# Kernel optimization log

Measured on AMD Instinct MI355X. Metric: run time of the kernel, lower is better.

Reference implementation:

```python
import jax, jax.numpy as jnp
import numpy as np

DIM = 1024
HEADS = 16
D_HEAD = 64
INNER = HEADS * D_HEAD  # 1024
CTX_DIM = 768
FF_INNER = 4 * DIM  # 4096
EPS = 1e-5
SCALE = D_HEAD ** -0.5


def _layer_norm(x, g, b):
    m = jnp.mean(x, axis=-1, keepdims=True)
    v = jnp.mean(jnp.square(x - m), axis=-1, keepdims=True)
    return (x - m) * jax.lax.rsqrt(v + EPS) * g + b


def _attention(x, ctx, wq, wk, wv, wo, bo):
    B, S, _ = x.shape
    T = ctx.shape[1]
    # project and split heads -> [B, H, S, Dh]
    q = (x @ wq).reshape(B, S, HEADS, D_HEAD).transpose(0, 2, 1, 3)
    k = (ctx @ wk).reshape(B, T, HEADS, D_HEAD).transpose(0, 2, 1, 3)
    v = (ctx @ wv).reshape(B, T, HEADS, D_HEAD).transpose(0, 2, 1, 3)
    attn = jnp.einsum('bhid,bhjd->bhij', q, k) * SCALE
    attn = jax.nn.softmax(attn, axis=-1)
    out = jnp.einsum('bhij,bhjd->bhid', attn, v)  # [B, H, S, Dh]
    out = out.transpose(0, 2, 1, 3).reshape(B, S, INNER)
    return out @ wo + bo


def setup_inputs() -> dict:
    key = jax.random.key(0)
    ks = jax.random.split(key, 20)
    rn = lambda k, shape, s=0.02: jax.random.normal(k, shape, dtype=jnp.float32) * s
    inp = {
        'hidden_states': jax.random.normal(ks[0], (4, 2048, DIM), dtype=jnp.float32),
        'context': jax.random.normal(ks[1], (4, 77, CTX_DIM), dtype=jnp.float32),
        # self-attention
        'wq1': rn(ks[2], (DIM, INNER)), 'wk1': rn(ks[3], (DIM, INNER)),
        'wv1': rn(ks[4], (DIM, INNER)),
        'wo1': rn(ks[5], (INNER, DIM)), 'bo1': jnp.zeros((DIM,), jnp.float32),
        # cross-attention (k/v from context dim 768)
        'wq2': rn(ks[6], (DIM, INNER)), 'wk2': rn(ks[7], (CTX_DIM, INNER)),
        'wv2': rn(ks[8], (CTX_DIM, INNER)),
        'wo2': rn(ks[9], (INNER, DIM)), 'bo2': jnp.zeros((DIM,), jnp.float32),
        # GEGLU feed-forward
        'w_ff1': rn(ks[10], (DIM, 2 * FF_INNER)), 'b_ff1': jnp.zeros((2 * FF_INNER,), jnp.float32),
        'w_ff2': rn(ks[11], (FF_INNER, DIM)), 'b_ff2': jnp.zeros((DIM,), jnp.float32),
        # layer norms
        'ln1_g': jnp.ones((DIM,), jnp.float32), 'ln1_b': jnp.zeros((DIM,), jnp.float32),
        'ln2_g': jnp.ones((DIM,), jnp.float32), 'ln2_b': jnp.zeros((DIM,), jnp.float32),
        'ln3_g': jnp.ones((DIM,), jnp.float32), 'ln3_b': jnp.zeros((DIM,), jnp.float32),
    }
    return inp


def reference(hidden_states, context, wq1, wk1, wv1, wo1, bo1,
              wq2, wk2, wv2, wo2, bo2, w_ff1, b_ff1, w_ff2, b_ff2,
              ln1_g, ln1_b, ln2_g, ln2_b, ln3_g, ln3_b):
    # self-attention, pre-norm residual
    h = hidden_states
    h = h + _attention(_layer_norm(h, ln1_g, ln1_b), _layer_norm(h, ln1_g, ln1_b),
                       wq1, wk1, wv1, wo1, bo1)
    # cross-attention
    h = h + _attention(_layer_norm(h, ln2_g, ln2_b), context,
                       wq2, wk2, wv2, wo2, bo2)
    # GEGLU feed-forward
    x = _layer_norm(h, ln3_g, ln3_b) @ w_ff1 + b_ff1
    lin, gate = jnp.split(x, 2, axis=2)
    h = h + (lin * jax.nn.gelu(gate)) @ w_ff2 + b_ff2
    return h
```

## Files before the change

### kernel.cpp

```cpp
#include <hip/hip_runtime.h>

#define DIMM 1024
#define NHEADS 16
#define DHEAD 64
#define BATCH 4
#define SEQ 2048
#define TCTX 77
#define CTXD 768
#define FFI 4096

typedef float f32x4 __attribute__((ext_vector_type(4)));
typedef __bf16 bf16x8 __attribute__((ext_vector_type(8)));

__device__ __forceinline__ float bf2f(unsigned short u){
  union { unsigned int i; float f; } c; c.i = ((unsigned int)u) << 16; return c.f;
}
__device__ __forceinline__ unsigned short f2bf(float f){
  union { float f; unsigned int i; } c; c.f = f;
  unsigned int i = c.i;
  return (unsigned short)((i + 0x7fffu + ((i >> 16) & 1u)) >> 16);
}
__device__ __forceinline__ void cp16(const unsigned short* g, unsigned short* l){
  __builtin_amdgcn_global_load_lds(
      (const __attribute__((address_space(1))) unsigned int*)g,
      (__attribute__((address_space(3))) unsigned int*)l, 16, 0, 0);
}

__global__ __launch_bounds__(256) void ln_kernel(const float* __restrict__ x,
                                                 const float* __restrict__ g,
                                                 const float* __restrict__ bb,
                                                 unsigned short* __restrict__ y)
{
  int row = blockIdx.x, tid = threadIdx.x;
  float4 raw = ((const float4*)(x + (size_t)row * DIMM))[tid];
  float v0 = raw.x, v1 = raw.y, v2 = raw.z, v3 = raw.w;
  float s  = v0 + v1 + v2 + v3;
  float sq = v0*v0 + v1*v1 + v2*v2 + v3*v3;
  #pragma unroll
  for (int off = 32; off; off >>= 1){ s += __shfl_xor(s, off); sq += __shfl_xor(sq, off); }
  __shared__ float sm[8];
  int wave = tid >> 6, lane = tid & 63;
  if (lane == 0){ sm[wave] = s; sm[4 + wave] = sq; }
  __syncthreads();
  s  = sm[0] + sm[1] + sm[2] + sm[3];
  sq = sm[4] + sm[5] + sm[6] + sm[7];
  float mean = s * (1.f / DIMM);
  float var  = sq * (1.f / DIMM) - mean * mean;
  float rstd = rsqrtf(var + 1e-5f);
  float4 gr = ((const float4*)g)[tid];
  float4 br = ((const float4*)bb)[tid];
  ushort4 o;
  o.x = f2bf((v0 - mean) * rstd * gr.x + br.x);
  o.y = f2bf((v1 - mean) * rstd * gr.y + br.y);
  o.z = f2bf((v2 - mean) * rstd * gr.z + br.z);
  o.w = f2bf((v3 - mean) * rstd * gr.w + br.w);
  ((ushort4*)(y + (size_t)row * DIMM))[tid] = o;
}

__global__ __launch_bounds__(256) void wt_kernel(const float* __restrict__ in,
                                                 unsigned short* __restrict__ out,
                                                 int K, int N)
{
  __shared__ float t[32][33];
  int tx = threadIdx.x & 31, ty = threadIdx.x >> 5;
  int k0 = blockIdx.y * 32, n0 = blockIdx.x * 32;
  #pragma unroll
  for (int i = 0; i < 4; i++)
    t[ty + i * 8][tx] = in[(size_t)(k0 + ty + i * 8) * N + n0 + tx];
  __syncthreads();
  #pragma unroll
  for (int i = 0; i < 4; i++)
    out[(size_t)(n0 + ty + i * 8) * K + k0 + tx] = f2bf(t[tx][ty + i * 8]);
}

#define CTXE (TCTX * BATCH * CTXD)
__global__ __launch_bounds__(256) void ctxcvt_kernel(const float* __restrict__ in,
                                                     unsigned short* __restrict__ out)
{
  int e = (blockIdx.x * 256 + threadIdx.x) * 4;
  float4 v;
  if (e < CTXE) v = *(const float4*)(in + e);
  else { v.x = 0.f; v.y = 0.f; v.z = 0.f; v.w = 0.f; }
  ushort4 o; o.x = f2bf(v.x); o.y = f2bf(v.y); o.z = f2bf(v.z); o.w = f2bf(v.w);
  *(ushort4*)(out + e) = o;
}

template<int RESF, int CF32>
__global__ __launch_bounds__(256) void gemm_bt(
    const unsigned short* __restrict__ A, int lda,
    const unsigned short* __restrict__ Bt, int ldb,
    const float* __restrict__ bias, const void* __restrict__ resv,
    void* __restrict__ Cv, int ldc,
    int M, int N, int K)
{
  __shared__ __align__(16) unsigned short As[128][64];
  __shared__ __align__(16) unsigned short Bs[128][64];
  int tid = threadIdx.x;
  int n0 = blockIdx.x * 128, row0 = blockIdx.y * 128;
  int wave = tid >> 6, lane = tid & 63, quad = lane >> 4, l16 = lane & 15;
  int wm = (wave >> 1) * 64, wn = (wave & 1) * 64;
  int wrow = wave * 32;
  int lrow = lane >> 3, lgrp = lane & 7;
  int gcol = ((lgrp ^ lrow) * 8);

  f32x4 acc[4][4];
  #pragma unroll
  for (int mt = 0; mt < 4; mt++)
    #pragma unroll
    for (int nt = 0; nt < 4; nt++) acc[mt][nt] = 0.f;

  for (int k0 = 0; k0 < K; k0 += 64) {
    const unsigned short* ga = A  + (size_t)(row0 + wrow + lrow) * lda + k0 + gcol;
    const unsigned short* gb = Bt + (size_t)(n0  + wrow + lrow) * ldb + k0 + gcol;
    #pragma unroll
    for (int i = 0; i < 4; i++){
      cp16(ga + (size_t)(8 * i) * lda, &As[wrow + 8 * i][0]);
      cp16(gb + (size_t)(8 * i) * ldb, &Bs[wrow + 8 * i][0]);
    }
    __syncthreads();
    #pragma unroll
    for (int kc = 0; kc < 2; kc++){
      bf16x8 af[4], bf[4];
      #pragma unroll
      for (int mt = 0; mt < 4; mt++){
        int R = wm + mt * 16 + l16;
        af[mt] = *(const bf16x8*)&As[R][((kc * 4 + quad) ^ (R & 7)) * 8];
      }
      #pragma unroll
      for (int nt = 0; nt < 4; nt++){
        int R = wn + nt * 16 + l16;
        bf[nt] = *(const bf16x8*)&Bs[R][((kc * 4 + quad) ^ (R & 7)) * 8];
      }
      #pragma unroll
      for (int mt = 0; mt < 4; mt++)
        #pragma unroll
        for (int nt = 0; nt < 4; nt++)
          acc[mt][nt] = __builtin_amdgcn_mfma_f32_16x16x32_bf16(af[mt], bf[nt], acc[mt][nt], 0, 0, 0);
    }
    __syncthreads();
  }

  #pragma unroll
  for (int nt = 0; nt < 4; nt++){
    int c = n0 + wn + nt * 16 + l16;
    float bv = bias ? bias[c] : 0.f;
    #pragma unroll
    for (int mt = 0; mt < 4; mt++){
      int rbase = row0 + wm + mt * 16 + quad * 4;
      #pragma unroll
      for (int rr = 0; rr < 4; rr++){
        int r = rbase + rr;
        if (r < M) {
          float val = acc[mt][nt][rr] + bv;
          size_t idx = (size_t)r * ldc + c;
          if (RESF) val += ((const float*)resv)[idx];
          if (CF32) ((float*)Cv)[idx] = val;
          else      ((unsigned short*)Cv)[idx] = f2bf(val);
        }
      }
    }
  }
}

__global__ __launch_bounds__(256) void ff1_geglu_bt(
    const unsigned short* __restrict__ A,
    const unsigned short* __restrict__ BtW,
    const float* __restrict__ bias,
    unsigned short* __restrict__ Z, int M)
{
  __shared__ __align__(16) unsigned short As[128][64];
  __shared__ __align__(16) unsigned short BsL[128][64];
  __shared__ __align__(16) unsigned short BsG[128][64];
  int tid = threadIdx.x;
  int n0 = blockIdx.x * 128, row0 = blockIdx.y * 128;
  int wave = tid >> 6, lane = tid & 63, quad = lane >> 4, l16 = lane & 15;
  int wm = (wave >> 1) * 64, wn = (wave & 1) * 64;
  int wrow = wave * 32;
  int lrow = lane >> 3, lgrp = lane & 7;
  int gcol = ((lgrp ^ lrow) * 8);

  f32x4 accL[4][4], accG[4][4];
  #pragma unroll
  for (int mt = 0; mt < 4; mt++)
    #pragma unroll
    for (int nt = 0; nt < 4; nt++){ accL[mt][nt] = 0.f; accG[mt][nt] = 0.f; }

  for (int k0 = 0; k0 < DIMM; k0 += 64) {
    const unsigned short* ga = A   + (size_t)(row0 + wrow + lrow) * DIMM + k0 + gcol;
    const unsigned short* gl = BtW + (size_t)(n0  + wrow + lrow) * DIMM + k0 + gcol;
    const unsigned short* gg = BtW + (size_t)(FFI + n0 + wrow + lrow) * DIMM + k0 + gcol;
    #pragma unroll
    for (int i = 0; i < 4; i++){
      cp16(ga + (size_t)(8 * i) * DIMM, &As[wrow + 8 * i][0]);
      cp16(gl + (size_t)(8 * i) * DIMM, &BsL[wrow + 8 * i][0]);
      cp16(gg + (size_t)(8 * i) * DIMM, &BsG[wrow + 8 * i][0]);
    }
    __syncthreads();
    #pragma unroll
    for (int kc = 0; kc < 2; kc++){
      bf16x8 af[4], b[4];
      #pragma unroll
      for (int mt = 0; mt < 4; mt++){
        int R = wm + mt * 16 + l16;
        af[mt] = *(const bf16x8*)&As[R][((kc * 4 + quad) ^ (R & 7)) * 8];
      }
      #pragma unroll
      for (int nt = 0; nt < 4; nt++){
        int R = wn + nt * 16 + l16;
        b[nt] = *(const bf16x8*)&BsL[R][((kc * 4 + quad) ^ (R & 7)) * 8];
      }
      #pragma unroll
      for (int mt = 0; mt < 4; mt++)
        #pragma unroll
        for (int nt = 0; nt < 4; nt++)
          accL[mt][nt] = __builtin_amdgcn_mfma_f32_16x16x32_bf16(af[mt], b[nt], accL[mt][nt], 0, 0, 0);
      #pragma unroll
      for (int nt = 0; nt < 4; nt++){
        int R = wn + nt * 16 + l16;
        b[nt] = *(const bf16x8*)&BsG[R][((kc * 4 + quad) ^ (R & 7)) * 8];
      }
      #pragma unroll
      for (int mt = 0; mt < 4; mt++)
        #pragma unroll
        for (int nt = 0; nt < 4; nt++)
          accG[mt][nt] = __builtin_amdgcn_mfma_f32_16x16x32_bf16(af[mt], b[nt], accG[mt][nt], 0, 0, 0);
    }
    __syncthreads();
  }

  #pragma unroll
  for (int nt = 0; nt < 4; nt++){
    int c = n0 + wn + nt * 16 + l16;
    float bvL = bias[c];
    float bvG = bias[c + FFI];
    #pragma unroll
    for (int mt = 0; mt < 4; mt++){
      int rbase = row0 + wm + mt * 16 + quad * 4;
      #pragma unroll
      for (int rr = 0; rr < 4; rr++){
        float lin = accL[mt][nt][rr] + bvL;
        float g   = accG[mt][nt][rr] + bvG;
        float y = 0.7978845608028654f * (g + 0.044715f * g * g * g);
        float e = __builtin_amdgcn_exp2f(y * 2.8853900817779268f);
        float t = 1.f - 2.f * __builtin_amdgcn_rcpf(e + 1.f);
        Z[(size_t)(rbase + rr) * FFI + c] = f2bf(lin * 0.5f * g * (1.f + t));
      }
    }
  }
}

__global__ __launch_bounds__(256) void attn_mfma(
    const unsigned short* __restrict__ Q, int ldq,
    const unsigned short* __restrict__ Kb,
    const unsigned short* __restrict__ Vb, int ldkv,
    unsigned short* __restrict__ O,
    int S, int T, float scale)
{
  int tid = threadIdx.x, wave = tid >> 6, lane = tid & 63;
  int quad = lane >> 4, l16 = lane & 15;
  int bh = blockIdx.y, b = bh >> 4, h = bh & 15;
  int qw = blockIdx.x * 128 + wave * 32;

  __shared__ __align__(16) unsigned short Ks[64][72];
  __shared__ __align__(16) unsigned short Vt[64][72];

  float qs = scale * 1.44269504088896f;
  bf16x8 Qf[2][2];
  #pragma unroll
  for (int mt = 0; mt < 2; mt++)
    #pragma unroll
    for (int kc = 0; kc < 2; kc++){
      const unsigned short* qp = Q + ((size_t)b * S + qw + mt * 16 + l16) * ldq
                                   + h * DHEAD + kc * 32 + quad * 8;
      union { float4 v; unsigned short u[8]; } ld; ld.v = *(const float4*)qp;
      union { bf16x8 v; unsigned short u[8]; } sc;
      #pragma unroll
      for (int j = 0; j < 8; j++) sc.u[j] = f2bf(bf2f(ld.u[j]) * qs);
      Qf[mt][kc] = sc.v;
    }

  f32x4 Oacc[2][4];
  float lp[2] = {0.f, 0.f};
  #pragma unroll
  for (int mt = 0; mt < 2; mt++)
    #pragma unroll
    for (int nt = 0; nt < 4; nt++) Oacc[mt][nt] = 0.f;

  for (int j0 = 0; j0 < T; j0 += 64){
    #pragma unroll
    for (int p = 0; p < 2; p++){
      int key = p * 32 + (tid >> 3);
      int d0 = (tid & 7) * 8;
      float4 kv;
      if (j0 + key < T) kv = *(const float4*)(Kb + ((size_t)b * T + j0 + key) * ldkv + h * DHEAD + d0);
      else { kv.x = 0.f; kv.y = 0.f; kv.z = 0.f; kv.w = 0.f; }
      *(float4*)&Ks[key][d0] = kv;
    }
    {
      int j = tid & 63, dbs = (tid >> 6) * 16;
      if (j0 + j < T){
        union { float4 v; unsigned short u[8]; } v1, v2;
        const unsigned short* vp = Vb + ((size_t)b * T + j0 + j) * ldkv + h * DHEAD + dbs;
        v1.v = ((const float4*)vp)[0];
        v2.v = ((const float4*)vp)[1];
        #pragma unroll
        for (int u = 0; u < 8; u++){ Vt[dbs + u][j] = v1.u[u]; Vt[dbs + 8 + u][j] = v2.u[u]; }
      } else {
        #pragma unroll
        for (int u = 0; u < 8; u++){ Vt[dbs + u][j] = 0; Vt[dbs + 8 + u][j] = 0; }
      }
    }
    __syncthreads();

    bool tail = (j0 + 64 > T);

    union pfu { bf16x8 v; __bf16 e[8]; } pf[2][2];

    #pragma unroll
    for (int mt = 0; mt < 2; mt++){
      f32x4 sT[4];
      #pragma unroll
      for (int nt = 0; nt < 4; nt++){
        sT[nt] = 0.f;
        #pragma unroll
        for (int kc = 0; kc < 2; kc++){
          bf16x8 kf = *(const bf16x8*)&Ks[nt * 16 + l16][kc * 32 + quad * 8];
          sT[nt] = __builtin_amdgcn_mfma_f32_16x16x32_bf16(kf, Qf[mt][kc], sT[nt], 0, 0, 0);
        }
      }
      #pragma unroll
      for (int nt = 0; nt < 4; nt++)
        #pragma unroll
        for (int rr = 0; rr < 4; rr++){
          float sv = sT[nt][rr];
          if (tail && (j0 + nt * 16 + quad * 4 + rr) >= T) sv = -1e30f;
          float p = __builtin_amdgcn_exp2f(fminf(sv, 108.f));
          lp[mt] += p;
          pf[mt][nt >> 1].e[(nt & 1) * 4 + rr] = (__bf16)p;
        }
    }

    #pragma unroll
    for (int kc = 0; kc < 2; kc++)
      #pragma unroll
      for (int nt = 0; nt < 4; nt++){
        union { bf16x8 v; ushort4 u[2]; } vf;
        vf.u[0] = *(const ushort4*)&Vt[nt * 16 + l16][kc * 32 + quad * 4];
        vf.u[1] = *(const ushort4*)&Vt[nt * 16 + l16][kc * 32 + 16 + quad * 4];
        #pragma unroll
        for (int mt = 0; mt < 2; mt++)
          Oacc[mt][nt] = __builtin_amdgcn_mfma_f32_16x16x32_bf16(pf[mt][kc].v, vf.v, Oacc[mt][nt], 0, 0, 0);
      }
    __syncthreads();
  }

  #pragma unroll
  for (int mt = 0; mt < 2; mt++){
    float l = lp[mt];
    l += __shfl_xor(l, 16);
    l += __shfl_xor(l, 32);
    float inv[4];
    #pragma unroll
    for (int rr = 0; rr < 4; rr++)
      inv[rr] = 1.f / __shfl(l, quad * 4 + rr);
    #pragma unroll
    for (int nt = 0; nt < 4; nt++)
      #pragma unroll
      for (int rr = 0; rr < 4; rr++){
        size_t idx = ((size_t)b * S + qw + mt * 16 + quad * 4 + rr) * DIMM
                     + h * DHEAD + nt * 16 + l16;
        O[idx] = f2bf(Oacc[mt][nt][rr] * inv[rr]);
      }
  }
}

extern "C" void kernel_launch(void* const* d_in, const int* in_sizes, int n_in,
                              void* d_out, int out_size, void* d_ws, size_t ws_size,
                              hipStream_t stream)
{
  const float* h0   = (const float*)d_in[0];
  const float* ctx  = (const float*)d_in[1];
  const float* wq1  = (const float*)d_in[2];
  const float* wk1  = (const float*)d_in[3];
  const float* wv1  = (const float*)d_in[4];
  const float* wo1  = (const float*)d_in[5];
  const float* bo1  = (const float*)d_in[6];
  const float* wq2  = (const float*)d_in[7];
  const float* wk2  = (const float*)d_in[8];
  const float* wv2  = (const float*)d_in[9];
  const float* wo2  = (const float*)d_in[10];
  const float* bo2  = (const float*)d_in[11];
  const float* wff1 = (const float*)d_in[12];
  const float* bff1 = (const float*)d_in[13];
  const float* wff2 = (const float*)d_in[14];
  const float* bff2 = (const float*)d_in[15];
  const float* ln1g = (const float*)d_in[16];
  const float* ln1b = (const float*)d_in[17];
  const float* ln2g = (const float*)d_in[18];
  const float* ln2b = (const float*)d_in[19];
  const float* ln3g = (const float*)d_in[20];
  const float* ln3b = (const float*)d_in[21];

  unsigned short* wsp = (unsigned short*)d_ws;
  const size_t RD = (size_t)BATCH * SEQ * DIMM;
  unsigned short* xn  = wsp;
  unsigned short* qkv = wsp + RD;
  unsigned short* ar  = wsp + 4 * RD;
  unsigned short* zb  = qkv;
  float* hres = (float*)d_out;

  const size_t M1 = (size_t)1024 * 1024;
  const int ROWS = BATCH * SEQ;
  const int CROWS = BATCH * TCTX;
  const float scale = 0.125f;
  dim3 blk(256);
  dim3 attn_grid(SEQ / 128, BATCH * NHEADS);

  wt_kernel<<<dim3(32, 32), blk, 0, stream>>>(wq1, ar,          DIMM, DIMM);
  wt_kernel<<<dim3(32, 32), blk, 0, stream>>>(wk1, ar + M1,     DIMM, DIMM);
  wt_kernel<<<dim3(32, 32), blk, 0, stream>>>(wv1, ar + 2 * M1, DIMM, DIMM);
  wt_kernel<<<dim3(32, 32), blk, 0, stream>>>(wo1, ar + 3 * M1, DIMM, DIMM);
  ln_kernel<<<ROWS, blk, 0, stream>>>(h0, ln1g, ln1b, xn);
  gemm_bt<0,0><<<dim3(3072 / 128, ROWS / 128), blk, 0, stream>>>(
      xn, DIMM, ar, DIMM, nullptr, nullptr, qkv, 3072, ROWS, 3072, DIMM);
  attn_mfma<<<attn_grid, blk, 0, stream>>>(qkv, 3072, qkv + 1024, qkv + 2048, 3072, xn, SEQ, SEQ, scale);
  gemm_bt<1,1><<<dim3(DIMM / 128, ROWS / 128), blk, 0, stream>>>(
      xn, DIMM, ar + 3 * M1, DIMM, bo1, h0, hres, DIMM, ROWS, DIMM, DIMM);

  unsigned short* wq2T  = ar;
  unsigned short* wkv2T = ar + M1;
  unsigned short* wo2T  = ar + M1 + (size_t)2048 * CTXD;
  unsigned short* xc    = wo2T + M1;
  wt_kernel<<<dim3(32, 32), blk, 0, stream>>>(wq2, wq2T, DIMM, DIMM);
  wt_kernel<<<dim3(32, 24), blk, 0, stream>>>(wk2, wkv2T, CTXD, DIMM);
  wt_kernel<<<dim3(32, 24), blk, 0, stream>>>(wv2, wkv2T + (size_t)1024 * CTXD, CTXD, DIMM);
  wt_kernel<<<dim3(32, 32), blk, 0, stream>>>(wo2, wo2T, DIMM, DIMM);
  ctxcvt_kernel<<<(384 * CTXD / 4) / 256, blk, 0, stream>>>(ctx, xc);
  ln_kernel<<<ROWS, blk, 0, stream>>>(hres, ln2g, ln2b, xn);
  gemm_bt<0,0><<<dim3(DIMM / 128, ROWS / 128), blk, 0, stream>>>(
      xn, DIMM, wq2T, DIMM, nullptr, nullptr, qkv, DIMM, ROWS, DIMM, DIMM);
  unsigned short* kvc = qkv + RD;
  gemm_bt<0,0><<<dim3(2048 / 128, 3), blk, 0, stream>>>(
      xc, CTXD, wkv2T, CTXD, nullptr, nullptr, kvc, 2048, CROWS, 2048, CTXD);
  attn_mfma<<<attn_grid, blk, 0, stream>>>(qkv, 1024, kvc, kvc + 1024, 2048, xn, SEQ, TCTX, scale);
  gemm_bt<1,1><<<dim3(DIMM / 128, ROWS / 128), blk, 0, stream>>>(
      xn, DIMM, wo2T, DIMM, bo2, hres, hres, DIMM, ROWS, DIMM, DIMM);

  unsigned short* wff1T = ar;
  unsigned short* wff2T = ar + 8 * M1;
  wt_kernel<<<dim3(256, 32),  blk, 0, stream>>>(wff1, wff1T, DIMM, 2 * FFI);
  wt_kernel<<<dim3(32, 128),  blk, 0, stream>>>(wff2, wff2T, FFI, DIMM);
  ln_kernel<<<ROWS, blk, 0, stream>>>(hres, ln3g, ln3b, xn);
  for (int half = 0; half < 2; half++){
    int r0 = half * 4096;
    ff1_geglu_bt<<<dim3(FFI / 128, 4096 / 128), blk, 0, stream>>>(
        xn + (size_t)r0 * DIMM, wff1T, bff1, zb, 4096);
    gemm_bt<1,1><<<dim3(DIMM / 128, 4096 / 128), blk, 0, stream>>>(
        zb, FFI, wff2T, FFI, bff2, hres + (size_t)r0 * DIMM,
        hres + (size_t)r0 * DIMM, DIMM, 4096, DIMM, FFI);
  }
}
```

Measured before the change: 1.016 ms.

## Halve attention query tile per wave and swizzle K tile with direct LDS loads

Each wave now processes 16 query rows instead of 32, so the attention grid doubles and register use drops, allowing higher occupancy via launch bounds of 8 blocks. K tiles are loaded with direct global-to-LDS copies into an XOR-swizzled unpadded layout, with a fallback path for the partial tail tile. The tradeoff is that each staged K/V tile is reused by half as many query rows, which increases LDS fill traffic and barrier count per unit of work.

Result: no change. 1.022 ms (+0.6%).

```diff
diff --git a/kernel.cpp b/kernel.cpp
--- a/kernel.cpp
+++ b/kernel.cpp
@@ -249,7 +249,7 @@
   }
 }
 
-__global__ __launch_bounds__(256) void attn_mfma(
+__global__ __launch_bounds__(256, 8) void attn_mfma(
     const unsigned short* __restrict__ Q, int ldq,
     const unsigned short* __restrict__ Kb,
     const unsigned short* __restrict__ Vb, int ldkv,
@@ -259,42 +259,49 @@
   int tid = threadIdx.x, wave = tid >> 6, lane = tid & 63;
   int quad = lane >> 4, l16 = lane & 15;
   int bh = blockIdx.y, b = bh >> 4, h = bh & 15;
-  int qw = blockIdx.x * 128 + wave * 32;
-
-  __shared__ __align__(16) unsigned short Ks[64][72];
+  int qw = blockIdx.x * 64 + wave * 16;
+
+  __shared__ __align__(16) unsigned short Ks[64][64];
   __shared__ __align__(16) unsigned short Vt[64][72];
 
   float qs = scale * 1.44269504088896f;
-  bf16x8 Qf[2][2];
-  #pragma unroll
-  for (int mt = 0; mt < 2; mt++)
-    #pragma unroll
-    for (int kc = 0; kc < 2; kc++){
-      const unsigned short* qp = Q + ((size_t)b * S + qw + mt * 16 + l16) * ldq
-                                   + h * DHEAD + kc * 32 + quad * 8;
-      union { float4 v; unsigned short u[8]; } ld; ld.v = *(const float4*)qp;
-      union { bf16x8 v; unsigned short u[8]; } sc;
-      #pragma unroll
-      for (int j = 0; j < 8; j++) sc.u[j] = f2bf(bf2f(ld.u[j]) * qs);
-      Qf[mt][kc] = sc.v;
-    }
-
-  f32x4 Oacc[2][4];
-  float lp[2] = {0.f, 0.f};
-  #pragma unroll
-  for (int mt = 0; mt < 2; mt++)
-    #pragma unroll
-    for (int nt = 0; nt < 4; nt++) Oacc[mt][nt] = 0.f;
+  bf16x8 Qf[2];
+  #pragma unroll
+  for (int kc = 0; kc < 2; kc++){
+    const unsigned short* qp = Q + ((size_t)b * S + qw + l16) * ldq
+                                 + h * DHEAD + kc * 32 + quad * 8;
+    union { float4 v; unsigned short u[8]; } ld; ld.v = *(const float4*)qp;
+    union { bf16x8 v; unsigned short u[8]; } sc;
+    #pragma unroll
+    for (int j = 0; j < 8; j++) sc.u[j] = f2bf(bf2f(ld.u[j]) * qs);
+    Qf[kc] = sc.v;
+  }
+
+  f32x4 Oacc[4];
+  float lp = 0.f;
+  #pragma unroll
+  for (int nt = 0; nt < 4; nt++) Oacc[nt] = 0.f;
+
+  int lrow = lane >> 3, lgrp = lane & 7;
+  int gcol = (lgrp ^ lrow) * 8;
 
   for (int j0 = 0; j0 < T; j0 += 64){
-    #pragma unroll
-    for (int p = 0; p < 2; p++){
-      int key = p * 32 + (tid >> 3);
-      int d0 = (tid & 7) * 8;
-      float4 kv;
-      if (j0 + key < T) kv = *(const float4*)(Kb + ((size_t)b * T + j0 + key) * ldkv + h * DHEAD + d0);
-      else { kv.x = 0.f; kv.y = 0.f; kv.z = 0.f; kv.w = 0.f; }
-      *(float4*)&Ks[key][d0] = kv;
+    bool tail = (j0 + 64 > T);
+    if (!tail){
+      const unsigned short* gk = Kb + ((size_t)b * T + j0 + wave * 16 + lrow) * ldkv
+                                    + h * DHEAD + gcol;
+      cp16(gk,                      &Ks[wave * 16 + lrow][0]);
+      cp16(gk + (size_t)8 * ldkv,   &Ks[wave * 16 + 8 + lrow][0]);
+    } else {
+      #pragma unroll
+      for (int p = 0; p < 2; p++){
+        int key = p * 32 + (tid >> 3);
+        int g = tid & 7;
+        float4 kv;
+        if (j0 + key < T) kv = *(const float4*)(Kb + ((size_t)b * T + j0 + key) * ldkv + h * DHEAD + g * 8);
+        else { kv.x = 0.f; kv.y = 0.f; kv.z = 0.f; kv.w = 0.f; }
+        *(float4*)&Ks[key][(g ^ (key & 7)) * 8] = kv;
+      }
     }
     {
       int j = tid & 63, dbs = (tid >> 6) * 16;
@@ -312,20 +319,16 @@
     }
     __syncthreads();
 
-    bool tail = (j0 + 64 > T);
-
-    union pfu { bf16x8 v; __bf16 e[8]; } pf[2][2];
-
-    #pragma unroll
-    for (int mt = 0; mt < 2; mt++){
+    union pfu { bf16x8 v; __bf16 e[8]; } pf[2];
+    {
       f32x4 sT[4];
       #pragma unroll
       for (int nt = 0; nt < 4; nt++){
         sT[nt] = 0.f;
         #pragma unroll
         for (int kc = 0; kc < 2; kc++){
-          bf16x8 kf = *(const bf16x8*)&Ks[nt * 16 + l16][kc * 32 + quad * 8];
-          sT[nt] = __builtin_amdgcn_mfma_f32_16x16x32_bf16(kf, Qf[mt][kc], sT[nt], 0, 0, 0);
+          bf16x8 kf = *(const bf16x8*)&Ks[nt * 16 + l16][((kc * 4 + quad) ^ (l16 & 7)) * 8];
+          sT[nt] = __builtin_amdgcn_mfma_f32_16x16x32_bf16(kf, Qf[kc], sT[nt], 0, 0, 0);
         }
       }
       #pragma unroll
@@ -335,8 +338,8 @@
           float sv = sT[nt][rr];
           if (tail && (j0 + nt * 16 + quad * 4 + rr) >= T) sv = -1e30f;
           float p = __builtin_amdgcn_exp2f(fminf(sv, 108.f));
-          lp[mt] += p;
-          pf[mt][nt >> 1].e[(nt & 1) * 4 + rr] = (__bf16)p;
+          lp += p;
+          pf[nt >> 1].e[(nt & 1) * 4 + rr] = (__bf16)p;
         }
     }
 
@@ -347,31 +350,26 @@
         union { bf16x8 v; ushort4 u[2]; } vf;
         vf.u[0] = *(const ushort4*)&Vt[nt * 16 + l16][kc * 32 + quad * 4];
         vf.u[1] = *(const ushort4*)&Vt[nt * 16 + l16][kc * 32 + 16 + quad * 4];
-        #pragma unroll
-        for (int mt = 0; mt < 2; mt++)
-          Oacc[mt][nt] = __builtin_amdgcn_mfma_f32_16x16x32_bf16(pf[mt][kc].v, vf.v, Oacc[mt][nt], 0, 0, 0);
-      }
-    __syncthreads();
-  }
-
-  #pragma unroll
-  for (int mt = 0; mt < 2; mt++){
-    float l = lp[mt];
-    l += __shfl_xor(l, 16);
-    l += __shfl_xor(l, 32);
-    float inv[4];
-    #pragma unroll
-    for (int rr = 0; rr < 4; rr++)
-      inv[rr] = 1.f / __shfl(l, quad * 4 + rr);
-    #pragma unroll
-    for (int nt = 0; nt < 4; nt++)
-      #pragma unroll
-      for (int rr = 0; rr < 4; rr++){
-        size_t idx = ((size_t)b * S + qw + mt * 16 + quad * 4 + rr) * DIMM
-                     + h * DHEAD + nt * 16 + l16;
-        O[idx] = f2bf(Oacc[mt][nt][rr] * inv[rr]);
-      }
-  }
+        Oacc[nt] = __builtin_amdgcn_mfma_f32_16x16x32_bf16(pf[kc].v, vf.v, Oacc[nt], 0, 0, 0);
+      }
+    __syncthreads();
+  }
+
+  float l = lp;
+  l += __shfl_xor(l, 16);
+  l += __shfl_xor(l, 32);
+  float inv[4];
+  #pragma unroll
+  for (int rr = 0; rr < 4; rr++)
+    inv[rr] = 1.f / __shfl(l, quad * 4 + rr);
+  #pragma unroll
+  for (int nt = 0; nt < 4; nt++)
+    #pragma unroll
+    for (int rr = 0; rr < 4; rr++){
+      size_t idx = ((size_t)b * S + qw + quad * 4 + rr) * DIMM
+                   + h * DHEAD + nt * 16 + l16;
+      O[idx] = f2bf(Oacc[nt][rr] * inv[rr]);
+    }
 }
 
 extern "C" void kernel_launch(void* const* d_in, const int* in_sizes, int n_in,
@@ -414,7 +412,7 @@
   const int CROWS = BATCH * TCTX;
   const float scale = 0.125f;
   dim3 blk(256);
-  dim3 attn_grid(SEQ / 128, BATCH * NHEADS);
+  dim3 attn_grid(SEQ / 64, BATCH * NHEADS);
 
   wt_kernel<<<dim3(32, 32), blk, 0, stream>>>(wq1, ar,          DIMM, DIMM);
   wt_kernel<<<dim3(32, 32), blk, 0, stream>>>(wk1, ar + M1,     DIMM, DIMM);
```
